# Kernel tuning notes

Hardware: AMD Instinct MI355X
Metric: run time of the kernel (lower is better)

The kernel has to match this reference:

```python
import jax, jax.numpy as jnp
import numpy as np

B, C, T, F = 2, 1, 8640, 8
HID = 16
MIN_H, MAX_H = 4.0, 48.0
SAMPLES_PER_HOUR = 60.0 * 6.0  # 10-second sampling


def setup_inputs() -> dict:
    key = jax.random.key(0)
    k1, k2, k3, k4 = jax.random.split(key, 4)
    attenuation = jax.random.normal(k1, (B, C, T), dtype=jnp.float32) * 2.0 + 10.0
    metadata = jax.random.normal(k2, (B, F), dtype=jnp.float32)
    # window-predictor MLP params (Linear(F,16) -> ReLU -> Linear(16,1) -> Sigmoid)
    w1 = jax.random.normal(k3, (F, HID), dtype=jnp.float32) * 0.35
    b1 = jnp.zeros((HID,), jnp.float32)
    w2 = jax.random.normal(k4, (HID, 1), dtype=jnp.float32) * 0.25
    b2 = jnp.zeros((1,), jnp.float32)
    return {"attenuation": attenuation, "metadata": metadata,
            "w1": w1, "b1": b1, "w2": w2, "b2": b2}


def _max_window(metadata, w1, b1, w2, b2, time_samples):
    # Mirrors the torch window predictor; result is a concrete Python int
    # (torch uses .item(), so the window size is a shape, not a traced value).
    h = jax.nn.relu(metadata @ w1 + b1)
    factor = jax.nn.sigmoid(h @ w2 + b2)[:, 0]            # [B]
    hours = MIN_H + factor * (MAX_H - MIN_H)
    samples = (hours * SAMPLES_PER_HOUR).astype(jnp.int32)  # .long() truncation
    return min(int(jnp.max(samples)), time_samples)


def reference(attenuation, metadata, w1, b1, w2, b2):
    t = attenuation.shape[2]
    max_window = _max_window(metadata, w1, b1, w2, b2, t)
    pad = max_window // 2
    midx = (max_window - 1) // 2  # torch.median picks the LOWER middle element
    # replicate padding == torch 'replicate'
    x = jnp.pad(attenuation, ((0, 0), (0, 0), (pad, pad)), mode="edge")
    n_out = x.shape[2] - max_window + 1  # unfold count with step=1
    # sliding windows via gather: [B, C, n_out, W]
    idx = jnp.arange(n_out)[:, None] + jnp.arange(max_window)[None, :]
    windows = x[:, :, idx]
    # median over window dim (lower-middle element, matching torch.median)
    return jnp.sort(windows, axis=-1)[..., midx]
```

## Files before the change

kernel.cpp:

```cpp
#include <hip/hip_runtime.h>
#include <math.h>


__device__ __forceinline__ int bin_of(float x, float vmin, float scale, int NB) {
    int v = (int)((x - vmin) * scale);
    return v < 0 ? 0 : (v > NB - 1 ? NB - 1 : v);
}

__global__ void __launch_bounds__(1024) k_setup(
    const float* __restrict__ atten, const float* __restrict__ md,
    const float* __restrict__ w1, const float* __restrict__ b1,
    const float* __restrict__ w2, const float* __restrict__ b2,
    int* __restrict__ hdr_i, float* __restrict__ hdr_f,
    int T, int n_out, int nTot)
{
    __shared__ float smin[16], smax[16];
    int tid = threadIdx.x;
    float vmin = 3.0e38f, vmax = -3.0e38f;
    int n4 = nTot >> 2;
    const float4* a4 = (const float4*)atten;
    for (int i = tid; i < n4; i += 1024) {
        float4 x = a4[i];
        vmin = fminf(vmin, fminf(fminf(x.x, x.y), fminf(x.z, x.w)));
        vmax = fmaxf(vmax, fmaxf(fmaxf(x.x, x.y), fmaxf(x.z, x.w)));
    }
    for (int i = (n4 << 2) + tid; i < nTot; i += 1024) {
        float x = atten[i];
        vmin = fminf(vmin, x); vmax = fmaxf(vmax, x);
    }
    #pragma unroll
    for (int off = 1; off < 64; off <<= 1) {
        vmin = fminf(vmin, __shfl_xor(vmin, off));
        vmax = fmaxf(vmax, __shfl_xor(vmax, off));
    }
    if ((tid & 63) == 0) { smin[tid >> 6] = vmin; smax[tid >> 6] = vmax; }
    __syncthreads();
    if (tid < 64) {
        int lane = tid;
        float m1 = (lane < 16) ? smin[lane] : 3.0e38f;
        float m2 = (lane < 16) ? smax[lane] : -3.0e38f;
        #pragma unroll
        for (int off = 1; off < 16; off <<= 1) {
            m1 = fminf(m1, __shfl_xor(m1, off));
            m2 = fmaxf(m2, __shfl_xor(m2, off));
        }
        int samples = 0;
        if (lane < 32) {
            int b = lane >> 4, j = lane & 15;
            float acc = b1[j];
            #pragma unroll
            for (int f = 0; f < 8; ++f) acc += md[b * 8 + f] * w1[f * 16 + j];
            float h = fmaxf(acc, 0.0f);
            float p = h * w2[j];
            #pragma unroll
            for (int off = 1; off < 16; off <<= 1) p += __shfl_xor(p, off);
            float s = p + b2[0];
            float factor = 1.0f / (1.0f + expf(-s));
            float hours = 4.0f + factor * (48.0f - 4.0f);
            samples = (int)(hours * 360.0f);
        }
        #pragma unroll
        for (int off = 1; off < 64; off <<= 1) samples = max(samples, __shfl_xor(samples, off));
        int mw = min(samples, T);
        int want_even = (n_out == T + 1) ? 1 : 0;
        if ((((mw & 1) == 0) ? 1 : 0) != want_even) { if (mw < T) mw += 1; else mw -= 1; }
        if (mw < 1) mw = 1;
        if (lane == 0) {
            hdr_i[0] = mw;
            hdr_i[1] = mw >> 1;
            hdr_i[2] = (mw - 1) >> 1;
            hdr_f[3] = m1;
            hdr_f[4] = m2;
        }
    }
}

template<int NB>
__global__ void __launch_bounds__(256) k_hist(
    const float* __restrict__ atten, unsigned char* __restrict__ binIdx,
    unsigned short* __restrict__ tileCnt, const float* __restrict__ hdr_f,
    int T, int NTe)
{
    __shared__ unsigned int hist[4][NB];
    int wave = threadIdx.x >> 6;
    int lane = threadIdx.x & 63;
    int g = blockIdx.x * 4 + wave;
    bool valid = g < 2 * NTe;
    int b = g / NTe, tile = g - b * NTe;

    #pragma unroll
    for (int j = lane; j < NB; j += 64) hist[wave][j] = 0;
    __syncthreads();

    int t = tile * 64 + lane;
    if (valid && t < T) {
        float vmin = hdr_f[3], vmax = hdr_f[4];
        float scale = (float)NB / fmaxf(vmax - vmin, 1e-10f);
        float x = atten[(size_t)b * T + t];
        int v = bin_of(x, vmin, scale, NB);
        binIdx[(size_t)b * T + t] = (unsigned char)v;
        atomicAdd(&hist[wave][v], 1u);
    }
    __syncthreads();
    if (valid) {
        unsigned short* row = tileCnt + ((size_t)b * NTe + tile) * NB;
        #pragma unroll
        for (int j = lane; j < NB; j += 64) row[j] = (unsigned short)hist[wave][j];
    }
}

template<int NB>
__global__ void __launch_bounds__(64) k_cdf(
    const unsigned char* __restrict__ binIdx, const unsigned short* __restrict__ tileCnt,
    unsigned short* __restrict__ F, int T, int NTe, int NTr16)
{
    constexpr int VPL = NB / 64;
    int blk = blockIdx.x;
    int b = blk / NTr16, r = blk - b * NTr16;
    int lane = threadIdx.x;
    int v0 = lane * VPL;
    int t0 = r * 16;

    int eb = t0 >> 6;
    int lead = t0 & 63;

    int bs[VPL];
    #pragma unroll
    for (int kk = 0; kk < VPL; ++kk) bs[kk] = 0;
    int rmax = eb < NTe ? eb : NTe;

    if (VPL == 4) {
        const uint2* cb2 = (const uint2*)(tileCnt + (size_t)b * NTe * NB) + lane;
        const int stride = NB / 4;
        unsigned ax[8], ay[8];
        #pragma unroll
        for (int q = 0; q < 8; ++q) { ax[q] = 0u; ay[q] = 0u; }
        int rp = 0;
        for (; rp + 8 <= rmax; rp += 8) {
            #pragma unroll
            for (int q = 0; q < 8; ++q) {
                uint2 u = cb2[(size_t)(rp + q) * stride];
                ax[q] += u.x; ay[q] += u.y;
            }
        }
        for (; rp < rmax; ++rp) {
            uint2 u = cb2[(size_t)rp * stride];
            ax[0] += u.x; ay[0] += u.y;
        }
        unsigned sx = 0, sy = 0;
        #pragma unroll
        for (int q = 0; q < 8; ++q) { sx += ax[q]; sy += ay[q]; }
        bs[0] = (int)(sx & 0xFFFFu); bs[1] = (int)(sx >> 16);
        bs[2] = (int)(sy & 0xFFFFu); bs[VPL - 1] = (int)(sy >> 16);
    } else {
        const unsigned short* cb = tileCnt + (size_t)b * NTe * NB + v0;
        int a[8];
        #pragma unroll
        for (int q = 0; q < 8; ++q) a[q] = 0;
        int rp = 0;
        for (; rp + 8 <= rmax; rp += 8) {
            #pragma unroll
            for (int q = 0; q < 8; ++q) a[q] += (int)cb[(size_t)(rp + q) * NB];
        }
        for (; rp < rmax; ++rp) a[0] += (int)cb[(size_t)rp * NB];
        #pragma unroll
        for (int q = 1; q < 8; ++q) a[0] += a[q];
        bs[0] = a[0];
    }

    int c[VPL];
    int loc = 0;
    #pragma unroll
    for (int kk = 0; kk < VPL; ++kk) { loc += bs[kk]; c[kk] = loc; }
    int incl = loc;
    #pragma unroll
    for (int off = 1; off < 64; off <<= 1) {
        int n = __shfl_up(incl, off);
        if (lane >= off) incl += n;
    }
    int excl = incl - loc;
    #pragma unroll
    for (int kk = 0; kk < VPL; ++kk) c[kk] += excl;

    const unsigned char* bi = binIdx + (size_t)b * T;

    int myLead = (lane < lead && (eb * 64 + lane) < T) ? (int)bi[eb * 64 + lane] : 0;
    for (int j = 0; j < lead; ++j) {
        int bt = __shfl(myLead, j);
        #pragma unroll
        for (int kk = 0; kk < VPL; ++kk) c[kk] += (v0 + kk >= bt) ? 1 : 0;
    }

    int t1 = min(T + 1, t0 + 16);
    int myb = (lane < 16 && (t0 + lane) < T) ? (int)bi[t0 + lane] : 0;
    unsigned short* Fb = F + (size_t)b * (T + 1) * NB;
    for (int t = t0; t < t1; ++t) {
        unsigned short* Ft = Fb + (size_t)t * NB + v0;
        if (VPL == 4) {
            uint2 pk;
            pk.x = (unsigned)c[0] | ((unsigned)c[1] << 16);
            pk.y = (unsigned)c[2] | ((unsigned)c[VPL - 1] << 16);
            *(uint2*)Ft = pk;
        } else {
            Ft[0] = (unsigned short)c[0];
        }
        if (t < T) {
            int bt = __shfl(myb, t - t0);
            #pragma unroll
            for (int kk = 0; kk < VPL; ++kk) c[kk] += (v0 + kk >= bt) ? 1 : 0;
        }
    }
}

template<int NB>
__global__ void __launch_bounds__(256) k_scatter(
    const float* __restrict__ atten, const unsigned char* __restrict__ binIdx,
    const unsigned short* __restrict__ F, float* __restrict__ bval, int T, int nTot)
{
    int i = blockIdx.x * 256 + threadIdx.x;
    if (i >= nTot) return;
    int b = i / T, t = i - b * T;
    int bn = binIdx[i];
    const unsigned short* Fb = F + (size_t)b * (T + 1) * NB;
    int s0   = bn ? (int)Fb[(size_t)T * NB + bn - 1] : 0;
    int FtB  = (int)Fb[(size_t)t * NB + bn];
    int FtP  = bn ? (int)Fb[(size_t)t * NB + bn - 1] : 0;
    bval[(size_t)b * T + (s0 + (FtB - FtP))] = atten[i];
}

template<int NB>
__global__ void __launch_bounds__(256) k_query(
    const float* __restrict__ atten, const unsigned short* __restrict__ F,
    const float* __restrict__ bval,
    const int* __restrict__ hdr_i, const float* __restrict__ hdr_f,
    float* __restrict__ out, int T, int n_out)
{
    constexpr int VPL = NB / 64;
    int wid = (blockIdx.x * 256 + threadIdx.x) >> 6;
    int lane = threadIdx.x & 63;
    if (wid >= 2 * n_out) return;
    int b = wid / n_out, o = wid - b * n_out;

    int mw = hdr_i[0], pad = hdr_i[1], k = hdr_i[2];
    float vmin = hdr_f[3], vmax = hdr_f[4];
    float range = fmaxf(vmax - vmin, 1e-10f);
    float binw = range / (float)NB;
    float scale = (float)NB / range;

    int lo_t = o - pad;
    int ta = max(lo_t, 0);
    int tb = min(lo_t + mw, T);
    int L  = ta - lo_t;
    int Rr = lo_t + mw - tb;

    const float* xb = atten + (size_t)b * T;
    float x0 = xb[0], xT = xb[T - 1];
    int b0 = bin_of(x0, vmin, scale, NB);
    int bT = bin_of(xT, vmin, scale, NB);

    const unsigned short* Fb = F + (size_t)b * (T + 1) * NB;
    int fa[VPL], fb[VPL];
    {
        const unsigned short* pa = Fb + (size_t)ta * NB + lane * VPL;
        const unsigned short* pb = Fb + (size_t)tb * NB + lane * VPL;
        if (VPL == 4) {
            uint2 ua = *(const uint2*)pa;
            fa[0] = (int)(ua.x & 0xFFFFu); fa[1] = (int)(ua.x >> 16);
            fa[2] = (int)(ua.y & 0xFFFFu); fa[VPL - 1] = (int)(ua.y >> 16);
            uint2 ub = *(const uint2*)pb;
            fb[0] = (int)(ub.x & 0xFFFFu); fb[1] = (int)(ub.x >> 16);
            fb[2] = (int)(ub.y & 0xFFFFu); fb[VPL - 1] = (int)(ub.y >> 16);
        } else {
            fa[0] = (int)pa[0]; fb[0] = (int)pb[0];
        }
    }

    int kk = k + 1;
    int w[VPL];
    #pragma unroll
    for (int j = 0; j < VPL; ++j) {
        int v = lane * VPL + j;
        w[j] = fb[j] - fa[j] + (b0 <= v ? L : 0) + (bT <= v ? Rr : 0);
    }
    unsigned long long m = __ballot(w[VPL - 1] >= kk);
    int ll = (int)__ffsll(m) - 1;

    int wj[VPL], faj[VPL], fbj[VPL];
    #pragma unroll
    for (int j = 0; j < VPL; ++j) {
        wj[j]  = __shfl(w[j], ll);
        faj[j] = __shfl(fa[j], ll);
        fbj[j] = __shfl(fb[j], ll);
    }
    int wprevL  = __shfl(w[VPL - 1], ll - 1);
    int faPrevL = __shfl(fa[VPL - 1], ll - 1);
    int fbPrevL = __shfl(fb[VPL - 1], ll - 1);
    if (ll == 0) { wprevL = 0; faPrevL = 0; fbPrevL = 0; }

    int jj = VPL - 1;
    #pragma unroll
    for (int j = VPL - 1; j >= 0; --j) if (wj[j] >= kk) jj = j;
    int bsel = ll * VPL + jj;
    int wprev = jj > 0 ? wj[jj - 1] : wprevL;
    int faSel = faj[jj], fbSel = fbj[jj];
    int pA = jj > 0 ? faj[jj - 1] : faPrevL;
    int pB = jj > 0 ? fbj[jj - 1] : fbPrevL;

    int kp = k - wprev;
    int withinA = faSel - pA;
    int cntw = (fbSel - pB) - withinA;
    int s0 = bsel ? (int)Fb[(size_t)T * NB + bsel - 1] : 0;
    int j0 = s0 + withinA;
    int j1e = j0 + cntw;

    int Lc = (b0 == bsel) ? L : 0;
    int Rc = (bT == bsel) ? Rr : 0;

    const float* bv = bval + (size_t)b * T;
    float vlo = vmin + (float)bsel * binw - binw;
    float vhi = vmin + (float)(bsel + 1) * binw + binw;

    const int CAND = 4;
    float rr[CAND];
    bool reg = (cntw <= 64 * CAND);
    if (reg) {
        #pragma unroll
        for (int q = 0; q < CAND; ++q) {
            int idx = j0 + lane + q * 64;
            rr[q] = (idx < j1e) ? bv[idx] : 3.0e38f;
        }
    }
    int need = kp + 1;
    for (int it = 0; it < 18; ++it) {
        float vm = 0.5f * (vlo + vhi);
        int cnt = ((x0 < vm) ? Lc : 0) + ((xT < vm) ? Rc : 0);
        if (reg) {
            #pragma unroll
            for (int q = 0; q < CAND; ++q)
                cnt += __popcll(__ballot(rr[q] < vm));
        } else {
            int my = 0;
            for (int j = j0 + lane; j < j1e; j += 64) my += (bv[j] < vm) ? 1 : 0;
            #pragma unroll
            for (int off = 1; off < 64; off <<= 1) my += __shfl_xor(my, off);
            cnt += my;
        }
        if (cnt >= need) vhi = vm; else vlo = vm;
    }
    if (lane == 0) out[(size_t)b * n_out + o] = 0.5f * (vlo + vhi);
}

__global__ void __launch_bounds__(256) k_fallback(
    const float* __restrict__ atten, const int* __restrict__ hdr_i,
    const float* __restrict__ hdr_f, float* __restrict__ out, int T, int n_out)
{
    int wave = threadIdx.x >> 6;
    int lane = threadIdx.x & 63;
    int gid = blockIdx.x * 4 + wave;
    if (gid >= 2 * n_out) return;
    int b = gid / n_out;
    int o = gid - b * n_out;
    int mw = hdr_i[0], pad = hdr_i[1], k = hdr_i[2];
    float lo = hdr_f[3] - 1e-3f, hi = hdr_f[4] + 1e-3f;
    const float* xb = atten + (size_t)b * T;
    int lo_t = o - pad;
    for (int it = 0; it < 26; ++it) {
        float vm = 0.5f * (lo + hi);
        int c = 0;
        for (int i = lane; i < mw; i += 64) {
            int t = lo_t + i;
            t = t < 0 ? 0 : (t >= T ? T - 1 : t);
            c += (xb[t] < vm) ? 1 : 0;
        }
        #pragma unroll
        for (int off = 1; off < 64; off <<= 1) c += __shfl_xor(c, off);
        if (c >= k + 1) hi = vm; else lo = vm;
    }
    if (lane == 0) out[(size_t)b * n_out + o] = 0.5f * (lo + hi);
}

struct Plan { size_t oBin, oCnt, oF, oV, total; };
static Plan make_plan(int NB, int nTot, int T, int NTe) {
    auto a64 = [](size_t x) { return (x + 63) & ~(size_t)63; };
    Plan p;
    size_t off = 64;
    p.oBin = off; off = a64(off + (size_t)nTot);
    p.oCnt = off; off = a64(off + (size_t)2 * NTe * NB * 2);
    p.oF   = off; off = a64(off + (size_t)2 * (T + 1) * NB * 2);
    p.oV   = off; off = a64(off + (size_t)nTot * 4);
    p.total = off;
    return p;
}

template<int NB>
static void run_pipeline(const float* atten, char* ws, const Plan& p,
                         const int* hdr_i, const float* hdr_f, float* out,
                         int T, int n_out, int nTot, int NTe,
                         hipStream_t stream)
{
    unsigned char*  binIdx  = (unsigned char*)(ws + p.oBin);
    unsigned short* tileCnt = (unsigned short*)(ws + p.oCnt);
    unsigned short* F       = (unsigned short*)(ws + p.oF);
    float*          bval    = (float*)(ws + p.oV);

    int NTr16 = (T + 1 + 15) / 16;
    int histBlocks = (2 * NTe + 3) / 4;
    k_hist<NB><<<dim3(histBlocks), dim3(256), 0, stream>>>(atten, binIdx, tileCnt, hdr_f, T, NTe);
    k_cdf<NB><<<dim3(2 * NTr16), dim3(64), 0, stream>>>(binIdx, tileCnt, F, T, NTe, NTr16);
    k_scatter<NB><<<dim3((nTot + 255) / 256), dim3(256), 0, stream>>>(atten, binIdx, F, bval, T, nTot);
    int nWaves = 2 * n_out;
    k_query<NB><<<dim3((nWaves + 3) / 4), dim3(256), 0, stream>>>(atten, F, bval, hdr_i, hdr_f, out, T, n_out);
}

extern "C" void kernel_launch(void* const* d_in, const int* in_sizes, int n_in,
                              void* d_out, int out_size, void* d_ws, size_t ws_size,
                              hipStream_t stream)
{
    const float* atten = (const float*)d_in[0];
    const float* md    = (const float*)d_in[1];
    const float* w1    = (const float*)d_in[2];
    const float* b1    = (const float*)d_in[3];
    const float* w2    = (const float*)d_in[4];
    const float* b2    = (const float*)d_in[5];
    float* out = (float*)d_out;

    const int B = 2;
    const int nTot  = in_sizes[0];
    const int T     = nTot / B;
    const int n_out = out_size / B;
    const int NTe = (T + 63) / 64;

    char* ws = (char*)d_ws;
    int*   hdr_i = (int*)ws;
    float* hdr_f = (float*)ws;

    k_setup<<<dim3(1), dim3(1024), 0, stream>>>(atten, md, w1, b1, w2, b2,
                                                hdr_i, hdr_f, T, n_out, nTot);

    Plan p256 = make_plan(256, nTot, T, NTe);
    Plan p64  = make_plan(64,  nTot, T, NTe);
    if (ws_size >= p256.total) {
        run_pipeline<256>(atten, ws, p256, hdr_i, hdr_f, out, T, n_out, nTot, NTe, stream);
    } else if (ws_size >= p64.total) {
        run_pipeline<64>(atten, ws, p64, hdr_i, hdr_f, out, T, n_out, nTot, NTe, stream);
    } else {
        int blocks = (2 * n_out + 3) / 4;
        k_fallback<<<dim3(blocks), dim3(256), 0, stream>>>(atten, hdr_i, hdr_f, out, T, n_out);
    }
}
```

Baseline: 104.5 us.

## Fuse CDF and scatter kernels, sample min/max, bound bisection by candidates

The scatter pass is merged into the CDF kernel. Each block now also sums the full per-tile histogram to get global bin offsets and writes every sample's value into its sorted-bin slot inline, so the separate k_scatter launch and its extra reads of F are gone. The setup kernel estimates the value range from a strided sample of 1024 elements on 256 threads instead of scanning the whole input; binning stays correct because out-of-range values are clamped. The query and fallback kernels take their bisection bounds from the actual candidate min/max rather than from bin edges, and the query runs 20 iterations. The trade-off is that the CDF kernel now reads every tile row instead of only the prefix, and sampled bounds can make bins less even.

```diff
diff --git a/kernel.cpp b/kernel.cpp
--- a/kernel.cpp
+++ b/kernel.cpp
@@ -7,26 +7,24 @@
     return v < 0 ? 0 : (v > NB - 1 ? NB - 1 : v);
 }
 
-__global__ void __launch_bounds__(1024) k_setup(
+__global__ void __launch_bounds__(256) k_setup(
     const float* __restrict__ atten, const float* __restrict__ md,
     const float* __restrict__ w1, const float* __restrict__ b1,
     const float* __restrict__ w2, const float* __restrict__ b2,
     int* __restrict__ hdr_i, float* __restrict__ hdr_f,
     int T, int n_out, int nTot)
 {
-    __shared__ float smin[16], smax[16];
+    __shared__ float smin[4], smax[4];
     int tid = threadIdx.x;
+    int strideS = nTot >> 10; if (strideS < 1) strideS = 1;
     float vmin = 3.0e38f, vmax = -3.0e38f;
-    int n4 = nTot >> 2;
-    const float4* a4 = (const float4*)atten;
-    for (int i = tid; i < n4; i += 1024) {
-        float4 x = a4[i];
-        vmin = fminf(vmin, fminf(fminf(x.x, x.y), fminf(x.z, x.w)));
-        vmax = fmaxf(vmax, fmaxf(fmaxf(x.x, x.y), fmaxf(x.z, x.w)));
-    }
-    for (int i = (n4 << 2) + tid; i < nTot; i += 1024) {
-        float x = atten[i];
-        vmin = fminf(vmin, x); vmax = fmaxf(vmax, x);
+    #pragma unroll
+    for (int q = 0; q < 4; ++q) {
+        int idx = (tid + q * 256) * strideS;
+        if (idx < nTot) {
+            float x = atten[idx];
+            vmin = fminf(vmin, x); vmax = fmaxf(vmax, x);
+        }
     }
     #pragma unroll
     for (int off = 1; off < 64; off <<= 1) {
@@ -37,10 +35,10 @@
     __syncthreads();
     if (tid < 64) {
         int lane = tid;
-        float m1 = (lane < 16) ? smin[lane] : 3.0e38f;
-        float m2 = (lane < 16) ? smax[lane] : -3.0e38f;
-        #pragma unroll
-        for (int off = 1; off < 16; off <<= 1) {
+        float m1 = (lane < 4) ? smin[lane] : 3.0e38f;
+        float m2 = (lane < 4) ? smax[lane] : -3.0e38f;
+        #pragma unroll
+        for (int off = 1; off < 4; off <<= 1) {
             m1 = fminf(m1, __shfl_xor(m1, off));
             m2 = fmaxf(m2, __shfl_xor(m2, off));
         }
@@ -110,9 +108,11 @@
 }
 
 template<int NB>
-__global__ void __launch_bounds__(64) k_cdf(
+__global__ void __launch_bounds__(64) k_cdf_scatter(
     const unsigned char* __restrict__ binIdx, const unsigned short* __restrict__ tileCnt,
-    unsigned short* __restrict__ F, int T, int NTe, int NTr16)
+    const float* __restrict__ atten,
+    unsigned short* __restrict__ F, float* __restrict__ bval,
+    int T, int NTe, int NTr16)
 {
     constexpr int VPL = NB / 64;
     int blk = blockIdx.x;
@@ -120,67 +120,94 @@
     int lane = threadIdx.x;
     int v0 = lane * VPL;
     int t0 = r * 16;
-
     int eb = t0 >> 6;
     int lead = t0 & 63;
 
-    int bs[VPL];
-    #pragma unroll
-    for (int kk = 0; kk < VPL; ++kk) bs[kk] = 0;
-    int rmax = eb < NTe ? eb : NTe;
-
+    int bs[VPL], ts[VPL];
     if (VPL == 4) {
         const uint2* cb2 = (const uint2*)(tileCnt + (size_t)b * NTe * NB) + lane;
         const int stride = NB / 4;
-        unsigned ax[8], ay[8];
-        #pragma unroll
-        for (int q = 0; q < 8; ++q) { ax[q] = 0u; ay[q] = 0u; }
+        unsigned bax[8], bay[8], tax[8], tay[8];
+        #pragma unroll
+        for (int q = 0; q < 8; ++q) { bax[q] = bay[q] = tax[q] = tay[q] = 0u; }
         int rp = 0;
-        for (; rp + 8 <= rmax; rp += 8) {
+        for (; rp + 8 <= NTe; rp += 8) {
             #pragma unroll
             for (int q = 0; q < 8; ++q) {
                 uint2 u = cb2[(size_t)(rp + q) * stride];
-                ax[q] += u.x; ay[q] += u.y;
+                bool inb = (rp + q) < eb;
+                tax[q] += u.x; tay[q] += u.y;
+                bax[q] += inb ? u.x : 0u; bay[q] += inb ? u.y : 0u;
             }
         }
-        for (; rp < rmax; ++rp) {
+        for (; rp < NTe; ++rp) {
             uint2 u = cb2[(size_t)rp * stride];
-            ax[0] += u.x; ay[0] += u.y;
-        }
-        unsigned sx = 0, sy = 0;
-        #pragma unroll
-        for (int q = 0; q < 8; ++q) { sx += ax[q]; sy += ay[q]; }
-        bs[0] = (int)(sx & 0xFFFFu); bs[1] = (int)(sx >> 16);
-        bs[2] = (int)(sy & 0xFFFFu); bs[VPL - 1] = (int)(sy >> 16);
+            bool inb = rp < eb;
+            tax[0] += u.x; tay[0] += u.y;
+            bax[0] += inb ? u.x : 0u; bay[0] += inb ? u.y : 0u;
+        }
+        unsigned bsx = 0, bsy = 0, tsx = 0, tsy = 0;
+        #pragma unroll
+        for (int q = 0; q < 8; ++q) { bsx += bax[q]; bsy += bay[q]; tsx += tax[q]; tsy += tay[q]; }
+        bs[0] = (int)(bsx & 0xFFFFu); bs[1] = (int)(bsx >> 16);
+        bs[2] = (int)(bsy & 0xFFFFu); bs[VPL - 1] = (int)(bsy >> 16);
+        ts[0] = (int)(tsx & 0xFFFFu); ts[1] = (int)(tsx >> 16);
+        ts[2] = (int)(tsy & 0xFFFFu); ts[VPL - 1] = (int)(tsy >> 16);
     } else {
         const unsigned short* cb = tileCnt + (size_t)b * NTe * NB + v0;
-        int a[8];
-        #pragma unroll
-        for (int q = 0; q < 8; ++q) a[q] = 0;
+        int ba[8], taq[8];
+        #pragma unroll
+        for (int q = 0; q < 8; ++q) { ba[q] = 0; taq[q] = 0; }
         int rp = 0;
-        for (; rp + 8 <= rmax; rp += 8) {
-            #pragma unroll
-            for (int q = 0; q < 8; ++q) a[q] += (int)cb[(size_t)(rp + q) * NB];
-        }
-        for (; rp < rmax; ++rp) a[0] += (int)cb[(size_t)rp * NB];
-        #pragma unroll
-        for (int q = 1; q < 8; ++q) a[0] += a[q];
-        bs[0] = a[0];
-    }
-
-    int c[VPL];
-    int loc = 0;
-    #pragma unroll
-    for (int kk = 0; kk < VPL; ++kk) { loc += bs[kk]; c[kk] = loc; }
-    int incl = loc;
-    #pragma unroll
-    for (int off = 1; off < 64; off <<= 1) {
-        int n = __shfl_up(incl, off);
-        if (lane >= off) incl += n;
-    }
-    int excl = incl - loc;
-    #pragma unroll
-    for (int kk = 0; kk < VPL; ++kk) c[kk] += excl;
+        for (; rp + 8 <= NTe; rp += 8) {
+            #pragma unroll
+            for (int q = 0; q < 8; ++q) {
+                int u = (int)cb[(size_t)(rp + q) * NB];
+                taq[q] += u;
+                ba[q] += ((rp + q) < eb) ? u : 0;
+            }
+        }
+        for (; rp < NTe; ++rp) {
+            int u = (int)cb[(size_t)rp * NB];
+            taq[0] += u;
+            ba[0] += (rp < eb) ? u : 0;
+        }
+        #pragma unroll
+        for (int q = 1; q < 8; ++q) { ba[0] += ba[q]; taq[0] += taq[q]; }
+        bs[0] = ba[0]; ts[0] = taq[0];
+    }
+
+    int c[VPL], totI[VPL];
+    {
+        int loc = 0;
+        #pragma unroll
+        for (int kk = 0; kk < VPL; ++kk) { loc += bs[kk]; c[kk] = loc; }
+        int incl = loc;
+        #pragma unroll
+        for (int off = 1; off < 64; off <<= 1) {
+            int n = __shfl_up(incl, off);
+            if (lane >= off) incl += n;
+        }
+        int excl = incl - loc;
+        #pragma unroll
+        for (int kk = 0; kk < VPL; ++kk) c[kk] += excl;
+    }
+    {
+        int loc = 0;
+        #pragma unroll
+        for (int kk = 0; kk < VPL; ++kk) { loc += ts[kk]; totI[kk] = loc; }
+        int incl = loc;
+        #pragma unroll
+        for (int off = 1; off < 64; off <<= 1) {
+            int n = __shfl_up(incl, off);
+            if (lane >= off) incl += n;
+        }
+        int excl = incl - loc;
+        #pragma unroll
+        for (int kk = 0; kk < VPL; ++kk) totI[kk] += excl;
+    }
+    int totLeft = __shfl_up(totI[VPL - 1], 1);
+    if (lane == 0) totLeft = 0;
 
     const unsigned char* bi = binIdx + (size_t)b * T;
 
@@ -192,8 +219,11 @@
     }
 
     int t1 = min(T + 1, t0 + 16);
-    int myb = (lane < 16 && (t0 + lane) < T) ? (int)bi[t0 + lane] : 0;
+    bool has16 = (lane < 16) && (t0 + lane) < T;
+    int   myb = has16 ? (int)bi[t0 + lane] : 0;
+    float myx = has16 ? atten[(size_t)b * T + t0 + lane] : 0.0f;
     unsigned short* Fb = F + (size_t)b * (T + 1) * NB;
+    float* bvb = bval + (size_t)b * T;
     for (int t = t0; t < t1; ++t) {
         unsigned short* Ft = Fb + (size_t)t * NB + v0;
         if (VPL == 4) {
@@ -205,27 +235,23 @@
             Ft[0] = (unsigned short)c[0];
         }
         if (t < T) {
-            int bt = __shfl(myb, t - t0);
+            int j = t - t0;
+            int bt = __shfl(myb, j);
+            float xv = __shfl(myx, j);
+            int cLeft = __shfl_up(c[VPL - 1], 1);
+            if (lane == 0) cLeft = 0;
+            int ow  = (VPL == 4) ? (bt >> 2) : bt;
+            int lc  = (VPL == 4) ? (bt & 3) : 0;
+            if (lane == ow) {
+                int prevc   = lc ? c[lc - 1]    : cLeft;
+                int within  = c[lc] - prevc;
+                int prevTot = lc ? totI[lc - 1] : totLeft;
+                bvb[prevTot + within] = xv;
+            }
             #pragma unroll
             for (int kk = 0; kk < VPL; ++kk) c[kk] += (v0 + kk >= bt) ? 1 : 0;
         }
     }
-}
-
-template<int NB>
-__global__ void __launch_bounds__(256) k_scatter(
-    const float* __restrict__ atten, const unsigned char* __restrict__ binIdx,
-    const unsigned short* __restrict__ F, float* __restrict__ bval, int T, int nTot)
-{
-    int i = blockIdx.x * 256 + threadIdx.x;
-    if (i >= nTot) return;
-    int b = i / T, t = i - b * T;
-    int bn = binIdx[i];
-    const unsigned short* Fb = F + (size_t)b * (T + 1) * NB;
-    int s0   = bn ? (int)Fb[(size_t)T * NB + bn - 1] : 0;
-    int FtB  = (int)Fb[(size_t)t * NB + bn];
-    int FtP  = bn ? (int)Fb[(size_t)t * NB + bn - 1] : 0;
-    bval[(size_t)b * T + (s0 + (FtB - FtP))] = atten[i];
 }
 
 template<int NB>
@@ -243,9 +269,7 @@
 
     int mw = hdr_i[0], pad = hdr_i[1], k = hdr_i[2];
     float vmin = hdr_f[3], vmax = hdr_f[4];
-    float range = fmaxf(vmax - vmin, 1e-10f);
-    float binw = range / (float)NB;
-    float scale = (float)NB / range;
+    float scale = (float)NB / fmaxf(vmax - vmin, 1e-10f);
 
     int lo_t = o - pad;
     int ta = max(lo_t, 0);
@@ -317,21 +341,40 @@
     int Rc = (bT == bsel) ? Rr : 0;
 
     const float* bv = bval + (size_t)b * T;
-    float vlo = vmin + (float)bsel * binw - binw;
-    float vhi = vmin + (float)(bsel + 1) * binw + binw;
 
     const int CAND = 4;
     float rr[CAND];
     bool reg = (cntw <= 64 * CAND);
+    float cmin = 3.0e38f, cmax = -3.0e38f;
     if (reg) {
         #pragma unroll
         for (int q = 0; q < CAND; ++q) {
             int idx = j0 + lane + q * 64;
-            rr[q] = (idx < j1e) ? bv[idx] : 3.0e38f;
-        }
-    }
+            if (idx < j1e) {
+                float v = bv[idx];
+                rr[q] = v;
+                cmin = fminf(cmin, v); cmax = fmaxf(cmax, v);
+            } else {
+                rr[q] = 3.0e38f;
+            }
+        }
+    } else {
+        for (int j = j0 + lane; j < j1e; j += 64) {
+            float v = bv[j];
+            cmin = fminf(cmin, v); cmax = fmaxf(cmax, v);
+        }
+    }
+    #pragma unroll
+    for (int off = 1; off < 64; off <<= 1) {
+        cmin = fminf(cmin, __shfl_xor(cmin, off));
+        cmax = fmaxf(cmax, __shfl_xor(cmax, off));
+    }
+    if (Lc > 0) { cmin = fminf(cmin, x0); cmax = fmaxf(cmax, x0); }
+    if (Rc > 0) { cmin = fminf(cmin, xT); cmax = fmaxf(cmax, xT); }
+
+    float vlo = cmin, vhi = cmax;
     int need = kp + 1;
-    for (int it = 0; it < 18; ++it) {
+    for (int it = 0; it < 20; ++it) {
         float vm = 0.5f * (vlo + vhi);
         int cnt = ((x0 < vm) ? Lc : 0) + ((xT < vm) ? Rc : 0);
         if (reg) {
@@ -352,7 +395,7 @@
 
 __global__ void __launch_bounds__(256) k_fallback(
     const float* __restrict__ atten, const int* __restrict__ hdr_i,
-    const float* __restrict__ hdr_f, float* __restrict__ out, int T, int n_out)
+    float* __restrict__ out, int T, int n_out)
 {
     int wave = threadIdx.x >> 6;
     int lane = threadIdx.x & 63;
@@ -361,9 +404,20 @@
     int b = gid / n_out;
     int o = gid - b * n_out;
     int mw = hdr_i[0], pad = hdr_i[1], k = hdr_i[2];
-    float lo = hdr_f[3] - 1e-3f, hi = hdr_f[4] + 1e-3f;
     const float* xb = atten + (size_t)b * T;
     int lo_t = o - pad;
+    float lo = 3.0e38f, hi = -3.0e38f;
+    for (int i = lane; i < mw; i += 64) {
+        int t = lo_t + i;
+        t = t < 0 ? 0 : (t >= T ? T - 1 : t);
+        float x = xb[t];
+        lo = fminf(lo, x); hi = fmaxf(hi, x);
+    }
+    #pragma unroll
+    for (int off = 1; off < 64; off <<= 1) {
+        lo = fminf(lo, __shfl_xor(lo, off));
+        hi = fmaxf(hi, __shfl_xor(hi, off));
+    }
     for (int it = 0; it < 26; ++it) {
         float vm = 0.5f * (lo + hi);
         int c = 0;
@@ -406,8 +460,7 @@
     int NTr16 = (T + 1 + 15) / 16;
     int histBlocks = (2 * NTe + 3) / 4;
     k_hist<NB><<<dim3(histBlocks), dim3(256), 0, stream>>>(atten, binIdx, tileCnt, hdr_f, T, NTe);
-    k_cdf<NB><<<dim3(2 * NTr16), dim3(64), 0, stream>>>(binIdx, tileCnt, F, T, NTe, NTr16);
-    k_scatter<NB><<<dim3((nTot + 255) / 256), dim3(256), 0, stream>>>(atten, binIdx, F, bval, T, nTot);
+    k_cdf_scatter<NB><<<dim3(2 * NTr16), dim3(64), 0, stream>>>(binIdx, tileCnt, atten, F, bval, T, NTe, NTr16);
     int nWaves = 2 * n_out;
     k_query<NB><<<dim3((nWaves + 3) / 4), dim3(256), 0, stream>>>(atten, F, bval, hdr_i, hdr_f, out, T, n_out);
 }
@@ -434,8 +487,8 @@
     int*   hdr_i = (int*)ws;
     float* hdr_f = (float*)ws;
 
-    k_setup<<<dim3(1), dim3(1024), 0, stream>>>(atten, md, w1, b1, w2, b2,
-                                                hdr_i, hdr_f, T, n_out, nTot);
+    k_setup<<<dim3(1), dim3(256), 0, stream>>>(atten, md, w1, b1, w2, b2,
+                                               hdr_i, hdr_f, T, n_out, nTot);
 
     Plan p256 = make_plan(256, nTot, T, NTe);
     Plan p64  = make_plan(64,  nTot, T, NTe);
@@ -445,6 +498,6 @@
         run_pipeline<64>(atten, ws, p64, hdr_i, hdr_f, out, T, n_out, nTot, NTe, stream);
     } else {
         int blocks = (2 * n_out + 3) / 4;
-        k_fallback<<<dim3(blocks), dim3(256), 0, stream>>>(atten, hdr_i, hdr_f, out, T, n_out);
-    }
-}
+        k_fallback<<<dim3(blocks), dim3(256), 0, stream>>>(atten, hdr_i, out, T, n_out);
+    }
+}
```

Measured after the change: 104.7 us. Within noise of the previous version (+0.2%).
